# Performance work log

Hardware: AMD Instinct MI355X
Metric: run time of the kernel (lower is better)

## Reference

```python
import jax, jax.numpy as jnp
import numpy as np

NE = 14  # NUM_ELEMENTS
CH = 18  # NE + density, gravity, fluid_momentum, cloner_assign
EMPTY, WALL, SAND, WATER, GAS, WOOD, ICE, FIRE, PLANT, STONE, LAVA, ACID, DUST, CLONER = range(14)
DENSITY = np.array([0., 5., 3., 2., -1., 5., 5., 0., 5., 4., 3., 2., 3., 5.], np.float32)
GRAVITY = np.array([1., 0., 1., 1., 1., 0., 1., 1., 0., 1., 1., 1., 1., 0.], np.float32)

# direction vectors for the 2-channel velocity field, layout [vy, vx]
UP = jnp.array([-1., 0.], jnp.float32).reshape(1, 2, 1, 1)
DOWN = jnp.array([1., 0.], jnp.float32).reshape(1, 2, 1, 1)
LEFT = jnp.array([0., -1.], jnp.float32).reshape(1, 2, 1, 1)
RIGHT = jnp.array([0., 1.], jnp.float32).reshape(1, 2, 1, 1)

get_above = lambda x: jnp.roll(x, 1, axis=2)
get_below = lambda x: jnp.roll(x, -1, axis=2)
get_left = lambda x: jnp.roll(x, 1, axis=3)
get_right = lambda x: jnp.roll(x, -1, axis=3)

def conv3x3(x):
    k = jnp.ones((1, 1, 3, 3), x.dtype)
    return jax.lax.conv_general_dilated(x, k, (1, 1), 'SAME',
        dimension_numbers=('NCHW', 'OIHW', 'NCHW'))

def get_bool(world, e):
    return world[:, e:e+1] == 1

def get_elem(world, e):
    return world[:, e:e+1]

def behavior_acid(world, rand_interact, elem_table):
    acid_rand = rand_interact < 0.2
    is_block = ~(get_bool(world, EMPTY) | get_bool(world, WALL) | get_bool(world, ACID) | get_bool(world, CLONER))
    is_acid = get_bool(world, ACID)
    does_acid = (is_acid & acid_rand & get_below(is_block)) | (is_acid & acid_rand & get_above(is_block))
    does_block = (is_block & get_above(acid_rand) & get_above(is_acid)) | (is_block & get_below(acid_rand) & get_below(is_acid))
    dd = does_acid | does_block
    empty_vec = elem_table[EMPTY].reshape(1, CH, 1, 1)
    return jnp.where(dd, empty_vec, world)

def behavior_fire(world, rand_interact, rand_element, velocity_field, elem_table):
    burn = rand_interact
    fire_and_lava = get_elem(world, FIRE) + get_elem(world, LAVA)
    has_fire_nb = conv3x3(fire_and_lava) > 0
    db_wood = get_bool(world, WOOD) & (burn < 0.05)
    db_plant = get_bool(world, PLANT) & (burn < 0.2)
    db_gas = get_bool(world, GAS) & (burn < 0.2)
    db_dust = get_bool(world, DUST)
    db_ice = get_bool(world, ICE) & (burn < 0.2) & has_fire_nb
    does_burn = (db_wood | db_plant | db_gas | db_dust) & has_fire_nb
    bfn = (does_burn & has_fire_nb).astype(world.dtype)
    dfn = (db_dust & has_fire_nb).astype(world.dtype)
    velocity_field = velocity_field - 2. * get_left(bfn) * LEFT - 2. * get_above(bfn) * UP \
        - 2. * get_below(bfn) * DOWN - 2. * get_right(bfn) * RIGHT \
        - 20. * get_left(dfn) * LEFT - 20. * get_above(dfn) * UP \
        - 20. * get_below(dfn) * DOWN - 20. * get_right(dfn) * RIGHT
    fire_vec = elem_table[FIRE].reshape(1, CH, 1, 1)
    water_vec = elem_table[WATER].reshape(1, CH, 1, 1)
    empty_vec = elem_table[EMPTY].reshape(1, CH, 1, 1)
    world = jnp.where(does_burn, fire_vec, world)
    world = jnp.where(db_ice, water_vec, world)
    burnables = get_elem(world, WOOD) + get_elem(world, PLANT) + get_elem(world, GAS) + get_elem(world, DUST)
    fire_with_burnable_nb = conv3x3(burnables) * fire_and_lava
    in_fire_range = conv3x3(fire_with_burnable_nb + get_elem(world, LAVA))
    db_empty = get_bool(world, EMPTY) & (in_fire_range > 0) & (burn < 0.3)
    world = jnp.where(db_empty, fire_vec, world)
    has_burnable_nb = conv3x3(burnables)
    fire_empty = get_bool(world, FIRE) & (rand_element < 0.4) & (has_burnable_nb == 0)
    world = jnp.where(fire_empty, empty_vec, world)
    return world, velocity_field

def behavior_fluid_flow(world, rand_movement, did_gravity):
    new_mom = jnp.zeros_like(world[:, :1])
    not_dg = did_gravity <= 0
    for elem in (EMPTY, WATER, GAS, LAVA, ACID):
        for fall_left in (True, False):
            fluid_mom = world[:, NE+2:NE+3]
            fall_dir = (rand_movement + fluid_mom + new_mom) > 0.5
            gdir = get_left if fall_left else get_right
            gnot = get_right if fall_left else get_left
            is_el = world[:, elem:elem+1] == 1
            is_r_el = gnot(is_el)
            density = world[:, NE:NE+1]
            is_match = fall_dir if fall_left else ~fall_dir
            is_r_match = gnot(is_match)
            l_dens_lo = (density - gdir(density)) > 0
            r_dens_hi = (gnot(density) - density) > 0
            is_grav = world[:, NE+1:NE+2] == 1
            l_grav = gdir(is_grav) & is_grav
            r_grav = gnot(is_grav) & is_grav
            dbl = is_match & is_el & not_dg & l_dens_lo & l_grav
            dbr = is_r_match & is_r_el & gnot(not_dg) & r_dens_hi & r_grav
            new_mom = new_mom + dbr * (2.0 if fall_left else -2.0)
            wl, wr = gdir(world), gnot(world)
            # interp2: (~a & ~b)*world + a*wl + b*wr (sums if both fire)
            world = (~(dbl | dbr)) * world + dbl * wl + dbr * wr
    return world.at[:, NE+2:NE+3].set(new_mom)

def behavior_cloner(world, elem_table):
    is_not_cloner = ~get_bool(world, CLONER)
    labels = jnp.argmax(world[:, :NE], axis=1)[:, None].astype(world.dtype)
    for gdir in (get_below, get_above, get_left, get_right):
        ca = world[:, NE+3:NE+4]
        is_cl_empty = get_bool(world, CLONER) & ((ca == 0) | (ca == 13))
        new_ca = (~(is_cl_empty | is_not_cloner)) * ca + is_cl_empty * gdir(labels)
        world = world.at[:, NE+3:NE+4].set(new_ca)
    ca = world[:, NE+3:NE+4]
    vec = elem_table[world[:, NE+3].astype(jnp.int32)]          # [B,H,W,CH]
    vec = jnp.transpose(vec, (0, 3, 1, 2))                       # [B,CH,H,W]
    is_cl_assigned = get_bool(world, CLONER) & ((ca != 0) & (ca != 13))
    for gdir in (get_below, get_above, get_left, get_right):
        is_dir = gdir(is_cl_assigned) & get_bool(world, EMPTY)
        world = jnp.where(is_dir, gdir(vec), world)
    return world

def make_elem_table():
    t = np.zeros((NE, CH), np.float32)
    t[np.arange(NE), np.arange(NE)] = 1.
    t[:, NE] = DENSITY
    t[:, NE+1] = GRAVITY
    return jnp.asarray(t)

def setup_inputs():
    key = jax.random.key(0)
    ks = jax.random.split(key, 5)
    B, H, W = 4, 512, 512
    elem_table = make_elem_table()
    ids = jax.random.randint(ks[0], (B, H, W), 0, NE)
    world = jnp.transpose(elem_table[ids], (0, 3, 1, 2))  # [B,CH,H,W]
    return {
        'world': world,
        'rand_movement': jax.random.uniform(ks[1], (B, 1, H, W), jnp.float32),
        'rand_interact': jax.random.uniform(ks[2], (B, 1, H, W), jnp.float32),
        'rand_element': jax.random.uniform(ks[3], (B, 1, H, W), jnp.float32),
        'velocity_field': jax.random.normal(ks[4], (B, 2, H, W), jnp.float32),
        'did_gravity': jnp.zeros((B, 1, H, W), jnp.float32),
        'elem_table': elem_table,
    }

def reference(world, rand_movement, rand_interact, rand_element, velocity_field, did_gravity, elem_table):
    world = behavior_acid(world, rand_interact, elem_table)
    world, velocity_field = behavior_fire(world, rand_interact, rand_element, velocity_field, elem_table)
    world = behavior_fluid_flow(world, rand_movement, did_gravity)
    world = behavior_cloner(world, elem_table)
    return world, velocity_field
```

## Files before the change

### kernel.cpp

```cpp
#include <hip/hip_runtime.h>

#define E_EMPTY  0
#define E_WALL   1
#define E_SAND   2
#define E_WATER  3
#define E_GAS    4
#define E_WOOD   5
#define E_ICE    6
#define E_FIRE   7
#define E_PLANT  8
#define E_STONE  9
#define E_LAVA   10
#define E_ACID   11
#define E_DUST   12
#define E_CLONER 13

#define CH 18
#define HW (512*512)
#define NPIX (4*HW)
#define NWORLD (4*CH*HW)

typedef unsigned long long u64;
#define ONE8 0x0101010101010101ULL
#define K7F  0x7F7F7F7F7F7F7F7FULL
#define H80  0x8080808080808080ULL
#define LOWN 0x0F0F0F0F0F0F0F0FULL

__constant__ float c_dens[14] = {0.f,5.f,3.f,2.f,-1.f,5.f,5.f,0.f,5.f,4.f,3.f,2.f,3.f,5.f};
__constant__ float c_grav[14] = {1.f,0.f,1.f,1.f,1.f,0.f,1.f,1.f,0.f,1.f,1.f,1.f,1.f,0.f};

__device__ __forceinline__ u64 bcast(int k) { return ONE8 * (unsigned)k; }
__device__ __forceinline__ u64 eqb(u64 x, int k) {
  u64 y = x ^ bcast(k);
  return ((~(y + K7F)) >> 7) & ONE8;
}
__device__ __forceinline__ u64 geb(u64 a, u64 b) { return (((a | H80) - b) >> 7) & ONE8; }
__device__ __forceinline__ u64 gtb(u64 a, u64 b) { return ONE8 ^ geb(b, a); }
__device__ __forceinline__ u64 mexp(u64 m) { return (m << 8) - m; }
__device__ __forceinline__ u64 fl01w(u64 e) { return eqb(e, E_FIRE) | eqb(e, E_LAVA); }
__device__ __forceinline__ u64 burn01w(u64 b) {
  u64 e = b & LOWN;
  return eqb(e,E_WOOD) | eqb(e,E_PLANT) | eqb(e,E_GAS) | eqb(e,E_DUST);
}
__device__ __forceinline__ u64 isblkw(u64 e) {
  return ONE8 ^ (eqb(e,E_EMPTY) | eqb(e,E_WALL) | eqb(e,E_ACID) | eqb(e,E_CLONER));
}

__device__ __forceinline__ unsigned char decode1(float d, float g, float f, float wa,
                                                 float wo, float pl, float sa, float lv, float wt) {
  if (g < 0.5f) {
    if (wa > 0.5f) return E_WALL;
    if (wo > 0.5f) return E_WOOD;
    if (pl > 0.5f) return E_PLANT;
    return E_CLONER;
  }
  int di = (int)d;
  if (di == 0) return (f > 0.5f) ? E_FIRE : E_EMPTY;
  if (di == 5) return E_ICE;
  if (di == 4) return E_STONE;
  if (di < 0)  return E_GAS;
  if (di == 3) { if (sa > 0.5f) return E_SAND; if (lv > 0.5f) return E_LAVA; return E_DUST; }
  return (wt > 0.5f) ? E_WATER : E_ACID;
}

__global__ __launch_bounds__(256) void k_prep(const float* __restrict__ w,
                                              const float* __restrict__ ri,
                                              const float* __restrict__ re,
                                              const float* __restrict__ rm,
                                              const float* __restrict__ dg,
                                              unsigned char* __restrict__ e0,
                                              unsigned char* __restrict__ rb) {
  int g = blockIdx.x * 256 + threadIdx.x;
  int base = g << 2;
  int b = base >> 18;
  int r = base & (HW - 1);
  const float* wb = w + (size_t)b * CH * HW + r;
  float4 D  = *reinterpret_cast<const float4*>(wb + (size_t)14 * HW);
  float4 G  = *reinterpret_cast<const float4*>(wb + (size_t)15 * HW);
  float4 F  = *reinterpret_cast<const float4*>(wb + (size_t)7  * HW);
  float4 WA = *reinterpret_cast<const float4*>(wb + (size_t)1  * HW);
  float4 WO = *reinterpret_cast<const float4*>(wb + (size_t)5  * HW);
  float4 PL = *reinterpret_cast<const float4*>(wb + (size_t)8  * HW);
  float4 SA = *reinterpret_cast<const float4*>(wb + (size_t)2  * HW);
  float4 LV = *reinterpret_cast<const float4*>(wb + (size_t)10 * HW);
  float4 WT = *reinterpret_cast<const float4*>(wb + (size_t)3  * HW);
  uchar4 e;
  e.x = decode1(D.x, G.x, F.x, WA.x, WO.x, PL.x, SA.x, LV.x, WT.x);
  e.y = decode1(D.y, G.y, F.y, WA.y, WO.y, PL.y, SA.y, LV.y, WT.y);
  e.z = decode1(D.z, G.z, F.z, WA.z, WO.z, PL.z, SA.z, LV.z, WT.z);
  e.w = decode1(D.w, G.w, F.w, WA.w, WO.w, PL.w, SA.w, LV.w, WT.w);
  *reinterpret_cast<uchar4*>(e0 + base) = e;

  float4 RI = *reinterpret_cast<const float4*>(ri + base);
  float4 RE = *reinterpret_cast<const float4*>(re + base);
  float4 RM = *reinterpret_cast<const float4*>(rm + base);
  float4 DG = *reinterpret_cast<const float4*>(dg + base);
  uchar4 q;
  q.x = (RI.x<0.05f?1:0)|(RI.x<0.2f?2:0)|(RI.x<0.3f?4:0)|(RE.x<0.4f?8:0)|(RM.x>0.5f?16:0)|(DG.x<=0.f?32:0);
  q.y = (RI.y<0.05f?1:0)|(RI.y<0.2f?2:0)|(RI.y<0.3f?4:0)|(RE.y<0.4f?8:0)|(RM.y>0.5f?16:0)|(DG.y<=0.f?32:0);
  q.z = (RI.z<0.05f?1:0)|(RI.z<0.2f?2:0)|(RI.z<0.3f?4:0)|(RE.z<0.4f?8:0)|(RM.z>0.5f?16:0)|(DG.z<=0.f?32:0);
  q.w = (RI.w<0.05f?1:0)|(RI.w<0.2f?2:0)|(RI.w<0.3f?4:0)|(RE.w<0.4f?8:0)|(RM.w>0.5f?16:0)|(DG.w<=0.f?32:0);
  *reinterpret_cast<uchar4*>(rb + base) = q;
}

__device__ __forceinline__ void fstep(bool left, int el, u64& E, u64& D, u64& Gv, u64& mom,
                                      u64 rmB, u64 ndB, u64 ndW, u64 ndE,
                                      int laneL, int laneR) {
  u64 fd = geb(mom, bcast(33)) | (eqb(mom, 32) & rmB);
  int pkT = (int)(E >> 56) | (((int)(D >> 56)) << 8) | (((int)(Gv >> 56)) << 11)
          | (((int)(fd >> 56)) << 12);
  int pkB = ((int)E & 255) | (((int)D & 255) << 8) | (((int)Gv & 1) << 11)
          | (((int)fd & 1) << 12);
  int pL = __shfl(pkT, laneL, 64);
  int pR = __shfl(pkB, laneR, 64);
  u64 EW = (E << 8) | (u64)(pL & 255);
  u64 DW = (D << 8) | (u64)((pL >> 8) & 7);
  u64 GW = (Gv << 8) | (u64)((pL >> 11) & 1);
  u64 EE = (E >> 8) | ((u64)(pR & 255) << 56);
  u64 DE = (D >> 8) | ((u64)((pR >> 8) & 7) << 56);
  u64 GE = (Gv >> 8) | ((u64)((pR >> 11) & 1) << 56);
  u64 dbl, dbr;
  if (left) {
    u64 fdE = (fd >> 8) | ((u64)((pR >> 12) & 1) << 56);
    dbl = fd  & eqb(E, el)  & ndB & gtb(D, DW) & GW & Gv;
    dbr = fdE & eqb(EE, el) & ndE & gtb(DE, D) & GE & Gv;
    mom += dbr << 1;
    u64 Ml = mexp(dbl), Mr = mexp(dbr), kp = ~(Ml | Mr);
    E  = (EW & Ml) | (EE & Mr) | (E  & kp);
    D  = (DW & Ml) | (DE & Mr) | (D  & kp);
    Gv = (GW & Ml) | (GE & Mr) | (Gv & kp);
  } else {
    u64 fdW = (fd << 8) | (u64)((pL >> 12) & 1);
    dbl = (fd  ^ ONE8) & eqb(E, el)  & ndB & gtb(D, DE) & GE & Gv;
    dbr = (fdW ^ ONE8) & eqb(EW, el) & ndW & gtb(DW, D) & GW & Gv;
    mom -= dbr << 1;
    u64 Ml = mexp(dbl), Mr = mexp(dbr), kp = ~(Ml | Mr);
    E  = (EE & Ml) | (EW & Mr) | (E  & kp);
    D  = (DE & Ml) | (DW & Mr) | (D  & kp);
    Gv = (GE & Ml) | (GW & Mr) | (Gv & kp);
  }
}

__global__ __launch_bounds__(512) void k_rest(const unsigned char* __restrict__ e0g,
                                              const unsigned char* __restrict__ rbg,
                                              const float* __restrict__ vin,
                                              float* __restrict__ out) {
  __shared__ u64 E0s[16][64];
  __shared__ u64 RBs[16][64];
  __shared__ u64 EASs[14][64];
  __shared__ u64 B1s[12][64];
  __shared__ u64 HBNs[10][64];
  __shared__ u64 ELs[8][64];
  __shared__ u64 nmsW[4][64];

  int tid = threadIdx.x;
  int blk = blockIdx.x;
  int b = blk >> 7;
  int ty = (blk & 127) << 2;
  int bbase = b * HW;
  float* vout = out + NWORLD;

  float vyR[4], vxR[4];
  #pragma unroll
  for (int r = 0; r < 4; ++r) {
    vyR[r] = vin[(size_t)(b*2+0)*HW + ((ty + r) << 9) + tid];
    vxR[r] = vin[(size_t)(b*2+1)*HW + ((ty + r) << 9) + tid];
  }

  {
    int l = tid >> 5, ch = (tid & 31) << 4;
    int gy = (ty + l - 6) & 511;
    int gi = bbase + (gy << 9) + ch;
    *reinterpret_cast<uint4*>(reinterpret_cast<char*>(&E0s[l][0]) + ch) =
        *reinterpret_cast<const uint4*>(e0g + gi);
    *reinterpret_cast<uint4*>(reinterpret_cast<char*>(&RBs[l][0]) + ch) =
        *reinterpret_cast<const uint4*>(rbg + gi);
  }
  __syncthreads();

  int w = tid & 63, rsl = tid >> 6;

  #pragma unroll
  for (int l = rsl; l < 14; l += 8) {
    u64 eu = E0s[l][w], ec = E0s[l+1][w], ed = E0s[l+2][w];
    u64 ru = RBs[l][w], rc = RBs[l+1][w], rd = RBs[l+2][w];
    u64 ibu = isblkw(eu), ibc = isblkw(ec), ibd = isblkw(ed);
    u64 da = eqb(ec,E_ACID) & ((rc>>1)&ONE8) & (ibd | ibu);
    u64 db = ibc & ((((ru>>1)&ONE8) & eqb(eu,E_ACID)) | (((rd>>1)&ONE8) & eqb(ed,E_ACID)));
    EASs[l][w] = ec & ~mexp(da | db);
  }
  __syncthreads();

  #pragma unroll
  for (int l = rsl; l < 12; l += 8) {
    int a = (ty + l - 4) & 511;
    u64 C1 = fl01w(EASs[l+1][w]);
    u64 L1 = w ? fl01w(EASs[l+1][w-1]) : 0;
    u64 R1 = (w < 63) ? fl01w(EASs[l+1][w+1]) : 0;
    u64 hf = C1 | (C1<<8) | (L1>>56) | (C1>>8) | (R1<<56);
    if (a != 0) {
      u64 C0 = fl01w(EASs[l][w]);
      u64 L0 = w ? fl01w(EASs[l][w-1]) : 0;
      u64 R0 = (w < 63) ? fl01w(EASs[l][w+1]) : 0;
      hf |= C0 | (C0<<8) | (L0>>56) | (C0>>8) | (R0<<56);
    }
    if (a != 511) {
      u64 C2 = fl01w(EASs[l+2][w]);
      u64 L2 = w ? fl01w(EASs[l+2][w-1]) : 0;
      u64 R2 = (w < 63) ? fl01w(EASs[l+2][w+1]) : 0;
      hf |= C2 | (C2<<8) | (L2>>56) | (C2>>8) | (R2<<56);
    }
    u64 e = EASs[l+1][w], rb = RBs[l+2][w];
    u64 m0 = rb & ONE8, m1 = (rb>>1) & ONE8;
    u64 eqd = eqb(e,E_DUST);
    u64 dbv = (eqb(e,E_WOOD)&m0) | (eqb(e,E_PLANT)&m1) | (eqb(e,E_GAS)&m1) | eqd;
    u64 burn = dbv & hf;
    u64 ice = eqb(e,E_ICE) & m1 & hf;
    u64 Mb = mexp(burn), Mi = mexp(ice) & ~Mb;
    u64 e1 = (bcast(E_FIRE) & Mb) | (bcast(E_WATER) & Mi) | (e & ~(Mb|Mi));
    B1s[l][w] = e1 | (burn<<4) | ((eqd & hf)<<5);
  }
  __syncthreads();

  #pragma unroll
  for (int l = rsl; l < 10; l += 8) {
    int a = (ty + l - 3) & 511;
    u64 C1 = burn01w(B1s[l+1][w]);
    u64 L1 = w ? burn01w(B1s[l+1][w-1]) : 0;
    u64 R1 = (w < 63) ? burn01w(B1s[l+1][w+1]) : 0;
    u64 s = C1 + ((C1<<8)|(L1>>56)) + ((C1>>8)|(R1<<56));
    if (a != 0) {
      u64 C0 = burn01w(B1s[l][w]);
      u64 L0 = w ? burn01w(B1s[l][w-1]) : 0;
      u64 R0 = (w < 63) ? burn01w(B1s[l][w+1]) : 0;
      s += C0 + ((C0<<8)|(L0>>56)) + ((C0>>8)|(R0<<56));
    }
    if (a != 511) {
      u64 C2 = burn01w(B1s[l+2][w]);
      u64 L2 = w ? burn01w(B1s[l+2][w-1]) : 0;
      u64 R2 = (w < 63) ? burn01w(B1s[l+2][w+1]) : 0;
      s += C2 + ((C2<<8)|(L2>>56)) + ((C2>>8)|(R2<<56));
    }
    HBNs[l][w] = s;
  }
  {
    const unsigned char* B1b = reinterpret_cast<const unsigned char*>(&B1s[0][0]);
    int x = tid;
    int xl1 = (x + 511) & 511, xr1 = (x + 1) & 511;
    #pragma unroll
    for (int r = 0; r < 4; ++r) {
      int gy = ty + r;
      int fu  = B1b[(r+3)*512 + x];
      int fd_ = B1b[(r+5)*512 + x];
      int flf = B1b[(r+4)*512 + xl1];
      int frt = B1b[(r+4)*512 + xr1];
      float vy = vyR[r];
      vy = vy + 2.0f*(float)((fu>>4)&1);   vy = vy - 2.0f*(float)((fd_>>4)&1);
      vy = vy + 20.0f*(float)((fu>>5)&1);  vy = vy - 20.0f*(float)((fd_>>5)&1);
      float vx = vxR[r];
      vx = vx + 2.0f*(float)((flf>>4)&1);  vx = vx - 2.0f*(float)((frt>>4)&1);
      vx = vx + 20.0f*(float)((flf>>5)&1); vx = vx - 20.0f*(float)((frt>>5)&1);
      vout[(size_t)(b*2+0)*HW + (gy<<9) + x] = vy;
      vout[(size_t)(b*2+1)*HW + (gy<<9) + x] = vx;
    }
  }
  __syncthreads();

  {
    int l = rsl;
    int a = (ty + l - 2) & 511;
    #define GW_(g, ww) ((HBNs[g][ww] & mexp(fl01w(EASs[(g)+2][ww]))) + eqb(B1s[(g)+1][ww] & LOWN, E_LAVA))
    u64 C1 = GW_(l+1, w);
    u64 L1 = w ? GW_(l+1, w-1) : 0;
    u64 R1 = (w < 63) ? GW_(l+1, w+1) : 0;
    u64 ifr = C1 + ((C1<<8)|(L1>>56)) + ((C1>>8)|(R1<<56));
    if (a != 0) {
      u64 C0 = GW_(l, w);
      u64 L0 = w ? GW_(l, w-1) : 0;
      u64 R0 = (w < 63) ? GW_(l, w+1) : 0;
      ifr += C0 + ((C0<<8)|(L0>>56)) + ((C0>>8)|(R0<<56));
    }
    if (a != 511) {
      u64 C2 = GW_(l+2, w);
      u64 L2 = w ? GW_(l+2, w-1) : 0;
      u64 R2 = (w < 63) ? GW_(l+2, w+1) : 0;
      ifr += C2 + ((C2<<8)|(L2>>56)) + ((C2>>8)|(R2<<56));
    }
    #undef GW_
    u64 nz = ((ifr + K7F) >> 7) & ONE8;
    u64 e1 = B1s[l+2][w] & LOWN;
    u64 rbW = RBs[l+4][w];
    u64 dbe = eqb(e1,E_EMPTY) & nz & ((rbW>>2)&ONE8);
    u64 e2 = e1 | (bcast(E_FIRE) & mexp(dbe));
    u64 fe = eqb(e2,E_FIRE) & ((rbW>>3)&ONE8) & eqb(HBNs[l+1][w], 0);
    u64 E = e2 & ~mexp(fe);

    u64 rmB = (rbW >> 4) & ONE8;
    u64 ndB = (rbW >> 5) & ONE8;
    u64 g1 = eqb(E,1), g5 = eqb(E,5), g8 = eqb(E,8), g13 = eqb(E,13);
    u64 m5 = g1|g5|eqb(E,6)|g8|g13;
    u64 m3 = eqb(E,2)|eqb(E,10)|eqb(E,12);
    u64 m2 = eqb(E,3)|eqb(E,11);
    u64 D = ONE8 + ((m5<<2)+m5) + ((m3<<1)+m3) + (m2<<1) + (eqb(E,9)<<2) - eqb(E,4);
    u64 Gv = ONE8 ^ (g1|g5|g8|g13);
    u64 mom = bcast(32);

    int lane = w;
    int laneL = (lane + 63) & 63, laneR = (lane + 1) & 63;
    int ndpk = (int)(ndB >> 56) | (((int)ndB & 1) << 1);
    u64 ndTopL = (u64)(__shfl(ndpk, laneL, 64) & 1);
    u64 ndBotR = (u64)((__shfl(ndpk, laneR, 64) >> 1) & 1);
    u64 ndW = (ndB << 8) | ndTopL;
    u64 ndE = (ndB >> 8) | (ndBotR << 56);

    #pragma unroll
    for (int ei = 0; ei < 5; ++ei) {
      const int el = (ei==0) ? E_EMPTY : (ei==1) ? E_WATER : (ei==2) ? E_GAS
                   : (ei==3) ? E_LAVA  : E_ACID;
      fstep(true,  el, E, D, Gv, mom, rmB, ndB, ndW, ndE, laneL, laneR);
      fstep(false, el, E, D, Gv, mom, rmB, ndB, ndW, ndE, laneL, laneR);
    }
    ELs[rsl][lane] = E;
    if (rsl >= 2 && rsl < 6) nmsW[rsl - 2][lane] = mom;
  }
  __syncthreads();

  {
    const unsigned char* ELb = reinterpret_cast<const unsigned char*>(&ELs[0][0]);
    const unsigned char* NMb = reinterpret_cast<const unsigned char*>(&nmsW[0][0]);
    int r = tid >> 7;
    int x0 = (tid & 127) << 2;
    const int DY[4] = {1, -1, 0, 0};
    const int DX[4] = {0, 0, -1, 1};
    int eo[4]; float mom[4], cao[4];
    #pragma unroll
    for (int k = 0; k < 4; ++k) {
      int xx = x0 + k;
      int ry = r + 2;
      int ec = ELb[ry*512 + xx];
      float m = (float)((int)NMb[r*512 + xx] - 32);
      int e = ec; float ca = 0.f;
      if (ec == E_CLONER) {
        int c = ELb[(ry+1)*512 + xx];
        if (c==0||c==13) c = ELb[(ry-1)*512 + xx];
        if (c==0||c==13) c = ELb[ry*512 + ((xx+511)&511)];
        if (c==0||c==13) c = ELb[ry*512 + ((xx+1)&511)];
        ca = (float)c;
      } else if (ec == E_EMPTY) {
        #pragma unroll
        for (int d = 0; d < 4; ++d) {
          int qy = ry + DY[d], qx = (xx + DX[d]) & 511;
          if (ELb[qy*512 + qx] == E_CLONER) {
            int c = ELb[(qy+1)*512 + qx];
            if (c==0||c==13) c = ELb[(qy-1)*512 + qx];
            if (c==0||c==13) c = ELb[qy*512 + ((qx+511)&511)];
            if (c==0||c==13) c = ELb[qy*512 + ((qx+1)&511)];
            if (c != 0 && c != 13) { e = c; m = 0.f; break; }
          }
        }
      }
      eo[k] = e; mom[k] = m; cao[k] = ca;
    }
    float* ob = out + (size_t)b * CH * HW + ((ty + r) << 9) + x0;
    #pragma unroll
    for (int c = 0; c < 14; ++c) {
      float4 v = make_float4(eo[0]==c ? 1.f : 0.f, eo[1]==c ? 1.f : 0.f,
                             eo[2]==c ? 1.f : 0.f, eo[3]==c ? 1.f : 0.f);
      *reinterpret_cast<float4*>(ob + (size_t)c * HW) = v;
    }
    *reinterpret_cast<float4*>(ob + (size_t)14*HW) =
        make_float4(c_dens[eo[0]], c_dens[eo[1]], c_dens[eo[2]], c_dens[eo[3]]);
    *reinterpret_cast<float4*>(ob + (size_t)15*HW) =
        make_float4(c_grav[eo[0]], c_grav[eo[1]], c_grav[eo[2]], c_grav[eo[3]]);
    *reinterpret_cast<float4*>(ob + (size_t)16*HW) =
        make_float4(mom[0], mom[1], mom[2], mom[3]);
    *reinterpret_cast<float4*>(ob + (size_t)17*HW) =
        make_float4(cao[0], cao[1], cao[2], cao[3]);
  }
}

extern "C" void kernel_launch(void* const* d_in, const int* in_sizes, int n_in,
                              void* d_out, int out_size, void* d_ws, size_t ws_size,
                              hipStream_t stream) {
  const float* world = (const float*)d_in[0];
  const float* rm    = (const float*)d_in[1];
  const float* ri    = (const float*)d_in[2];
  const float* re    = (const float*)d_in[3];
  const float* vel   = (const float*)d_in[4];
  const float* dg    = (const float*)d_in[5];
  float* out = (float*)d_out;

  char* ws = (char*)d_ws;
  unsigned char* e0 = (unsigned char*)ws;
  unsigned char* rb = e0 + NPIX;

  hipLaunchKernelGGL(k_prep, dim3(NPIX/1024), dim3(256), 0, stream,
                     world, ri, re, rm, dg, e0, rb);
  hipLaunchKernelGGL(k_rest, dim3(4*128), dim3(512), 0, stream,
                     e0, rb, vel, out);
}
```

Baseline: 43.63 us.

## Halve rows per block, double grid, split output channels across thread halves

Each block of k_rest now produces 2 output rows instead of 4, so the grid grows to 1024 blocks and more CUs get work. The staged halo shrinks to match, and the output stores are split so two groups of 256 threads each write 9 of the 18 channels. Blocks are also remapped with a stride-8 interleave, likely to spread adjacent tiles across XCDs. In exchange, the fixed 6-row halo is now loaded for only 2 output rows, so redundant loading and compute per output pixel roughly doubles, and some stencil stages leave threads idle.

```diff
diff --git a/kernel.cpp b/kernel.cpp
--- a/kernel.cpp
+++ b/kernel.cpp
@@ -145,29 +145,30 @@
                                               const unsigned char* __restrict__ rbg,
                                               const float* __restrict__ vin,
                                               float* __restrict__ out) {
-  __shared__ u64 E0s[16][64];
-  __shared__ u64 RBs[16][64];
-  __shared__ u64 EASs[14][64];
-  __shared__ u64 B1s[12][64];
-  __shared__ u64 HBNs[10][64];
-  __shared__ u64 ELs[8][64];
-  __shared__ u64 nmsW[4][64];
+  __shared__ u64 E0s[14][64];
+  __shared__ u64 RBs[14][64];
+  __shared__ u64 EASs[12][64];
+  __shared__ u64 B1s[10][64];
+  __shared__ u64 HBNs[8][64];
+  __shared__ u64 ELs[6][64];
+  __shared__ u64 nmsW[2][64];
 
   int tid = threadIdx.x;
-  int blk = blockIdx.x;
-  int b = blk >> 7;
-  int ty = (blk & 127) << 2;
+  int blk0 = blockIdx.x;
+  int blk = (blk0 & 7) * 128 + (blk0 >> 3);
+  int b = blk >> 8;
+  int ty = (blk & 255) << 1;
   int bbase = b * HW;
   float* vout = out + NWORLD;
 
-  float vyR[4], vxR[4];
+  float vyR[2], vxR[2];
   #pragma unroll
-  for (int r = 0; r < 4; ++r) {
+  for (int r = 0; r < 2; ++r) {
     vyR[r] = vin[(size_t)(b*2+0)*HW + ((ty + r) << 9) + tid];
     vxR[r] = vin[(size_t)(b*2+1)*HW + ((ty + r) << 9) + tid];
   }
 
-  {
+  if (tid < 448) {
     int l = tid >> 5, ch = (tid & 31) << 4;
     int gy = (ty + l - 6) & 511;
     int gi = bbase + (gy << 9) + ch;
@@ -181,7 +182,7 @@
   int w = tid & 63, rsl = tid >> 6;
 
   #pragma unroll
-  for (int l = rsl; l < 14; l += 8) {
+  for (int l = rsl; l < 12; l += 8) {
     u64 eu = E0s[l][w], ec = E0s[l+1][w], ed = E0s[l+2][w];
     u64 ru = RBs[l][w], rc = RBs[l+1][w], rd = RBs[l+2][w];
     u64 ibu = isblkw(eu), ibc = isblkw(ec), ibd = isblkw(ed);
@@ -192,7 +193,7 @@
   __syncthreads();
 
   #pragma unroll
-  for (int l = rsl; l < 12; l += 8) {
+  for (int l = rsl; l < 10; l += 8) {
     int a = (ty + l - 4) & 511;
     u64 C1 = fl01w(EASs[l+1][w]);
     u64 L1 = w ? fl01w(EASs[l+1][w-1]) : 0;
@@ -222,8 +223,8 @@
   }
   __syncthreads();
 
-  #pragma unroll
-  for (int l = rsl; l < 10; l += 8) {
+  {
+    int l = rsl;
     int a = (ty + l - 3) & 511;
     u64 C1 = burn01w(B1s[l+1][w]);
     u64 L1 = w ? burn01w(B1s[l+1][w-1]) : 0;
@@ -248,7 +249,7 @@
     int x = tid;
     int xl1 = (x + 511) & 511, xr1 = (x + 1) & 511;
     #pragma unroll
-    for (int r = 0; r < 4; ++r) {
+    for (int r = 0; r < 2; ++r) {
       int gy = ty + r;
       int fu  = B1b[(r+3)*512 + x];
       int fd_ = B1b[(r+5)*512 + x];
@@ -266,7 +267,7 @@
   }
   __syncthreads();
 
-  {
+  if (rsl < 6) {
     int l = rsl;
     int a = (ty + l - 2) & 511;
     #define GW_(g, ww) ((HBNs[g][ww] & mexp(fl01w(EASs[(g)+2][ww]))) + eqb(B1s[(g)+1][ww] & LOWN, E_LAVA))
@@ -321,15 +322,16 @@
       fstep(false, el, E, D, Gv, mom, rmB, ndB, ndW, ndE, laneL, laneR);
     }
     ELs[rsl][lane] = E;
-    if (rsl >= 2 && rsl < 6) nmsW[rsl - 2][lane] = mom;
+    if (rsl == 2 || rsl == 3) nmsW[rsl - 2][lane] = mom;
   }
   __syncthreads();
 
   {
     const unsigned char* ELb = reinterpret_cast<const unsigned char*>(&ELs[0][0]);
     const unsigned char* NMb = reinterpret_cast<const unsigned char*>(&nmsW[0][0]);
-    int r = tid >> 7;
-    int x0 = (tid & 127) << 2;
+    int q = tid & 255, h = tid >> 8;
+    int r = q >> 7;
+    int x0 = (q & 127) << 2;
     const int DY[4] = {1, -1, 0, 0};
     const int DX[4] = {0, 0, -1, 1};
     int eo[4]; float mom[4], cao[4];
@@ -362,20 +364,23 @@
       eo[k] = e; mom[k] = m; cao[k] = ca;
     }
     float* ob = out + (size_t)b * CH * HW + ((ty + r) << 9) + x0;
-    #pragma unroll
-    for (int c = 0; c < 14; ++c) {
-      float4 v = make_float4(eo[0]==c ? 1.f : 0.f, eo[1]==c ? 1.f : 0.f,
-                             eo[2]==c ? 1.f : 0.f, eo[3]==c ? 1.f : 0.f);
+    int c0 = h * 9, c1 = c0 + 9;
+    for (int c = c0; c < c1; ++c) {
+      float4 v;
+      if (c < 14) {
+        v = make_float4(eo[0]==c ? 1.f : 0.f, eo[1]==c ? 1.f : 0.f,
+                        eo[2]==c ? 1.f : 0.f, eo[3]==c ? 1.f : 0.f);
+      } else if (c == 14) {
+        v = make_float4(c_dens[eo[0]], c_dens[eo[1]], c_dens[eo[2]], c_dens[eo[3]]);
+      } else if (c == 15) {
+        v = make_float4(c_grav[eo[0]], c_grav[eo[1]], c_grav[eo[2]], c_grav[eo[3]]);
+      } else if (c == 16) {
+        v = make_float4(mom[0], mom[1], mom[2], mom[3]);
+      } else {
+        v = make_float4(cao[0], cao[1], cao[2], cao[3]);
+      }
       *reinterpret_cast<float4*>(ob + (size_t)c * HW) = v;
     }
-    *reinterpret_cast<float4*>(ob + (size_t)14*HW) =
-        make_float4(c_dens[eo[0]], c_dens[eo[1]], c_dens[eo[2]], c_dens[eo[3]]);
-    *reinterpret_cast<float4*>(ob + (size_t)15*HW) =
-        make_float4(c_grav[eo[0]], c_grav[eo[1]], c_grav[eo[2]], c_grav[eo[3]]);
-    *reinterpret_cast<float4*>(ob + (size_t)16*HW) =
-        make_float4(mom[0], mom[1], mom[2], mom[3]);
-    *reinterpret_cast<float4*>(ob + (size_t)17*HW) =
-        make_float4(cao[0], cao[1], cao[2], cao[3]);
   }
 }
 
@@ -396,6 +401,6 @@
 
   hipLaunchKernelGGL(k_prep, dim3(NPIX/1024), dim3(256), 0, stream,
                      world, ri, re, rm, dg, e0, rb);
-  hipLaunchKernelGGL(k_rest, dim3(4*128), dim3(512), 0, stream,
+  hipLaunchKernelGGL(k_rest, dim3(4*256), dim3(512), 0, stream,
                      e0, rb, vel, out);
 }
```

New measurement: 55.41 us. 27.0% more time.
